# Kernel tuning notes

Hardware: AMD Instinct MI355X
Metric: run time of the kernel (lower is better)

The kernel has to match this reference:

```python
import jax, jax.numpy as jnp
import numpy as np

B, S, HIDDEN = 2, 4096, 4096
NUM_HEADS = 32
QK_NOPE = 128
QK_ROPE = 64
QK_HEAD = QK_NOPE + QK_ROPE
KV_LORA = 512
Q_LORA = 1536


def setup_inputs() -> dict:
    key = jax.random.key(0)
    k1, k2, k3, k4, k5, k6 = jax.random.split(key, 6)
    x = jax.random.normal(k1, (B, S, HIDDEN), dtype=jnp.float32)
    cos = jax.random.uniform(k2, (B, S, QK_ROPE), dtype=jnp.float32)
    sin = jax.random.uniform(k3, (B, S, QK_ROPE), dtype=jnp.float32)
    # Linear weights, torch layout [out, in]
    Wqa = jax.random.normal(k4, (Q_LORA, HIDDEN), dtype=jnp.float32) * 0.02
    Wqb = jax.random.normal(k5, (NUM_HEADS * QK_HEAD, Q_LORA), dtype=jnp.float32) * 0.02
    Wkva = jax.random.normal(k6, (KV_LORA + QK_ROPE, HIDDEN), dtype=jnp.float32) * 0.02
    return {"x": x, "cos": cos, "sin": sin, "Wqa": Wqa, "Wqb": Wqb, "Wkva": Wkva}


def _rotate_half(t):
    d = t.shape[-1] // 2
    return jnp.concatenate([-t[..., d:], t[..., :d]], axis=-1)


def reference(x, cos, sin, Wqa, Wqb, Wkva):
    b, s, _ = x.shape
    # low-rank Q: x -> q_lora -> heads*(nope+rope)
    q = jnp.einsum('bsh,rh->bsr', x, Wqa)
    q = jnp.einsum('bsr,or->bso', q, Wqb).reshape(b, s, NUM_HEADS, QK_HEAD)
    q_nope = q[..., :QK_NOPE]
    q_pe = q[..., QK_NOPE:]
    # KV down-projection with MQA rope part
    kv = jnp.einsum('bsh,oh->bso', x, Wkva)
    compressed_kv = kv[..., :KV_LORA]                         # [b,s,kv_lora]
    k_pe = kv[..., KV_LORA:].reshape(b, s, 1, QK_ROPE)
    # NeoX explicit RoPE, unsqueeze_dim=2
    c = cos[:, :, None, :]
    sn = sin[:, :, None, :]
    q_pe_rot = q_pe * c + _rotate_half(q_pe) * sn
    k_pe_rot = k_pe * c + _rotate_half(k_pe) * sn
    q_out = jnp.concatenate([q_nope, q_pe_rot], axis=-1).reshape(b, s, -1)
    k_out = k_pe_rot.reshape(b, s, QK_ROPE)
    return jnp.concatenate([q_out, k_out, compressed_kv], axis=-1)
```

## Files before the change

kernel.cpp:

```cpp
#include <hip/hip_runtime.h>
#include <hip/hip_bf16.h>
#include <stdint.h>

typedef __bf16 bf16x8 __attribute__((ext_vector_type(8)));
typedef float f32x4 __attribute__((ext_vector_type(4)));
typedef float fvec4 __attribute__((ext_vector_type(4)));
typedef unsigned short usvec4 __attribute__((ext_vector_type(4)));
typedef unsigned int ui32x4 __attribute__((ext_vector_type(4)));

#define AS3 __attribute__((address_space(3)))
#define AS1 __attribute__((address_space(1)))

static __device__ __forceinline__ unsigned short f2bf(float f) {
  unsigned int u = __float_as_uint(f);
  u += 0x7FFF + ((u >> 16) & 1);
  return (unsigned short)(u >> 16);
}


extern "C" __global__ void cvt_bf16_kernel(const float* __restrict__ src,
                                           unsigned short* __restrict__ dst,
                                           long n4) {
  long i = (long)blockIdx.x * blockDim.x + threadIdx.x;
  const long stride = (long)gridDim.x * blockDim.x;
  for (; i < n4; i += stride) {
    const fvec4 v = __builtin_nontemporal_load(&((const fvec4*)src)[i]);
    usvec4 o;
    o.x = f2bf(v.x); o.y = f2bf(v.y); o.z = f2bf(v.z); o.w = f2bf(v.w);
    ((usvec4*)dst)[i] = o;
  }
}

extern "C" __global__ void cvt_pad_kernel(const float* __restrict__ src,
                                          unsigned short* __restrict__ dst,
                                          long nsrc4, long ntot4) {
  long i = (long)blockIdx.x * blockDim.x + threadIdx.x;
  const long stride = (long)gridDim.x * blockDim.x;
  for (; i < ntot4; i += stride) {
    usvec4 o = {0, 0, 0, 0};
    if (i < nsrc4) {
      const fvec4 v = __builtin_nontemporal_load(&((const fvec4*)src)[i]);
      o.x = f2bf(v.x); o.y = f2bf(v.y); o.z = f2bf(v.z); o.w = f2bf(v.w);
    }
    ((usvec4*)dst)[i] = o;
  }
}


#define VMW(N) asm volatile("s_waitcnt vmcnt(" #N ")" ::: "memory")
#define BAR() __builtin_amdgcn_s_barrier()
#define LGKM0() do { asm volatile("s_waitcnt lgkmcnt(0)" ::: "memory"); \
                     __builtin_amdgcn_sched_barrier(0); } while (0)

template <int MODE>
__global__ __launch_bounds__(512, 2)
void mla_gemm(const __hip_bfloat16* __restrict__ A0p,
              const __hip_bfloat16* __restrict__ B0p, int K0,
              const __hip_bfloat16* __restrict__ A1p,
              const __hip_bfloat16* __restrict__ B1p,
              unsigned short* __restrict__ qlora,
              const float* __restrict__ cosp,
              const float* __restrict__ sinp,
              float* __restrict__ out) {
  extern __shared__ __align__(128) char lds[];
  const int tid = threadIdx.x;
  const int lane = tid & 63;
  const int w = tid >> 6;
  const int wm = w >> 2, wn = w & 3;
  const int l15 = lane & 15, lhi = lane >> 4;
  const int srow8 = lane >> 3;
  const int swzc = ((lane & 7) ^ srow8) * 8;

  const __hip_bfloat16* Aptr;
  const __hip_bfloat16* Bptr;
  int K, bm, bn;
  bool isA2 = false;
  if constexpr (MODE == 0) {
    const int swz = ((int)blockIdx.x & 7) * 32 + ((int)blockIdx.x >> 3);
    bm = swz >> 3; bn = swz & 7;
    Aptr = A0p; Bptr = B0p; K = K0;
  } else {
    const int bid = (int)blockIdx.x;
    if (bid < 32) {
      isA2 = true; bm = bid; bn = 8; Aptr = A1p; Bptr = B1p; K = 4096;
    } else {
      const int b2 = bid - 32;
      const int swz = (b2 & 7) * 96 + (b2 >> 3);
      bm = swz / 24; bn = swz - bm * 24;
      Aptr = A0p; Bptr = B0p; K = K0;
    }
  }
  const long brow = (long)bm * 256;
  const int bcol = bn * 256;

  const __hip_bfloat16* aSt = Aptr + (brow + w * 16 + srow8) * (long)K + swzc;
  const __hip_bfloat16* bSt = Bptr + ((long)bcol + srow8) * (long)K + swzc;
  const int wj0 = w * 16, wj1 = w * 16 + 8;
  const int cb_j0 = (2 * (wj0 >> 5)) * 32 + (wj0 & 31);
  const int cb_j1 = (2 * (wj1 >> 5)) * 32 + (wj1 & 31);
  const int ldsWj = w * 2048;

  const int aRdRow = (wm * 64 + l15) * 128;
  const int bRdRow = (wn * 32 + l15) * 128;
  const int ck0 = (lhi ^ (l15 & 7)) * 16;

  f32x4 acc[8][4] = {};
  bf16x8 aF[4][2];
  bf16x8 bF[2][2][2];

  const int T = K >> 6;
  const int I = T >> 1;

  auto stage = [&](int u, int kt) {
    const int b = kt & 1;
    if (u < 2) {
      const int off = b * 32768 + u * 16384 + ldsWj;
      __builtin_amdgcn_global_load_lds((AS1 void*)(aSt + (long)(u * 128) * K + kt * 64),
                                       (AS3 void*)(lds + off), 16, 0, 0);
      __builtin_amdgcn_global_load_lds((AS1 void*)(aSt + (long)(u * 128 + 8) * K + kt * 64),
                                       (AS3 void*)(lds + off + 1024), 16, 0, 0);
    } else {
      const int h = u - 2;
      const int off = 65536 + b * 32768 + h * 16384 + ldsWj;
      __builtin_amdgcn_global_load_lds((AS1 void*)(bSt + (long)(cb_j0 + h * 32) * K + kt * 64),
                                       (AS3 void*)(lds + off), 16, 0, 0);
      __builtin_amdgcn_global_load_lds((AS1 void*)(bSt + (long)(cb_j1 + h * 32) * K + kt * 64),
                                       (AS3 void*)(lds + off + 1024), 16, 0, 0);
    }
  };
  auto readA = [&](int qh, int b) {
    const int base = b * 32768 + qh * 16384 + aRdRow;
    #pragma unroll
    for (int fr = 0; fr < 4; ++fr) {
      aF[fr][0] = *(const bf16x8*)(lds + base + fr * 2048 + ck0);
      aF[fr][1] = *(const bf16x8*)(lds + base + fr * 2048 + (ck0 ^ 64));
    }
  };
  auto readB = [&](int c, int b) {
    const int base = 65536 + b * 32768 + c * 16384 + bRdRow;
    #pragma unroll
    for (int fq = 0; fq < 2; ++fq) {
      bF[c][fq][0] = *(const bf16x8*)(lds + base + fq * 2048 + ck0);
      bF[c][fq][1] = *(const bf16x8*)(lds + base + fq * 2048 + (ck0 ^ 64));
    }
  };
  auto mmac = [&](int qh, int c) {
    __builtin_amdgcn_s_setprio(1);
    #pragma unroll
    for (int fr = 0; fr < 4; ++fr)
      #pragma unroll
      for (int fq = 0; fq < 2; ++fq) {
        acc[qh * 4 + fr][c * 2 + fq] = __builtin_amdgcn_mfma_f32_16x16x32_bf16(
            aF[fr][0], bF[c][fq][0], acc[qh * 4 + fr][c * 2 + fq], 0, 0, 0);
        acc[qh * 4 + fr][c * 2 + fq] = __builtin_amdgcn_mfma_f32_16x16x32_bf16(
            aF[fr][1], bF[c][fq][1], acc[qh * 4 + fr][c * 2 + fq], 0, 0, 0);
      }
    __builtin_amdgcn_s_setprio(0);
  };

  stage(0, 0); stage(2, 0); stage(3, 0); stage(1, 0);
  stage(0, 1); stage(2, 1); stage(3, 1); stage(1, 1);
  VMW(12);
  BAR();

  for (int i = 0; i < I - 1; ++i) {
    const int e2 = 2 * i + 2, o2 = 2 * i + 3;
    readA(0, 0); readB(0, 0);
    BAR(); LGKM0(); mmac(0, 0); VMW(10); BAR();
    readB(1, 0); stage(0, e2); stage(2, e2);
    BAR(); LGKM0(); mmac(0, 1); VMW(12); BAR();
    readA(1, 0); stage(3, e2);
    BAR(); LGKM0(); mmac(1, 1); BAR();
    stage(1, e2);
    BAR(); LGKM0(); mmac(1, 0); VMW(12); BAR();
    readA(0, 1); readB(0, 1);
    BAR(); LGKM0(); mmac(0, 0); VMW(10); BAR();
    readB(1, 1); stage(0, o2); stage(2, o2);
    BAR(); LGKM0(); mmac(0, 1); VMW(12); BAR();
    readA(1, 1); stage(3, o2);
    BAR(); LGKM0(); mmac(1, 1); BAR();
    stage(1, o2);
    BAR(); LGKM0(); mmac(1, 0); VMW(12); BAR();
  }
  readA(0, 0); readB(0, 0);
  BAR(); LGKM0(); mmac(0, 0); VMW(10); BAR();
  readB(1, 0);
  BAR(); LGKM0(); mmac(0, 1); VMW(8); BAR();
  readA(1, 0);
  BAR(); LGKM0(); mmac(1, 1); BAR();
  BAR(); LGKM0(); mmac(1, 0); VMW(4); BAR();
  readA(0, 1); readB(0, 1);
  BAR(); LGKM0(); mmac(0, 0); VMW(2); BAR();
  readB(1, 1);
  BAR(); LGKM0(); mmac(0, 1); VMW(0); BAR();
  readA(1, 1);
  BAR(); LGKM0(); mmac(1, 1); BAR();
  BAR(); LGKM0(); mmac(1, 0); BAR();

  const int wcol = bcol + wn * 64;
  const long rbase = brow + wm * 64;
  char* eplds = lds + w * 4096;

  auto storeTileF32 = [&](int i8, float* dst, bool rope) {
    #pragma unroll
    for (int j = 0; j < 4; ++j)
      #pragma unroll
      for (int r = 0; r < 4; ++r) {
        float v = acc[i8][j][r];
        if (rope) {
          const long row = rbase + (i8 >> 2) * 128 + (i8 & 3) * 16 + lhi * 4 + r;
          const int d = (j >> 1) * 32 + (j & 1) * 16 + l15;
          const float rot = (j < 2) ? -acc[i8][j + 2][r] : acc[i8][j - 2][r];
          v = v * cosp[row * 64 + d] + rot * sinp[row * 64 + d];
        }
        *(float*)(eplds + (lhi * 4 + r) * 256 + ((j >> 1) * 32 + (j & 1) * 16 + l15) * 4) = v;
      }
    asm volatile("s_waitcnt lgkmcnt(0)" ::: "memory");
    #pragma unroll
    for (int t = 0; t < 4; ++t) {
      const int r16 = t * 4 + (lane >> 4);
      const f32x4 v = *(const f32x4*)(eplds + r16 * 256 + (lane & 15) * 16);
      const long row = rbase + (i8 >> 2) * 128 + (i8 & 3) * 16 + r16;
      __builtin_nontemporal_store(v, (f32x4*)(dst + row * 6720 + (lane & 15) * 4));
    }
  };
  auto storeTileBf16 = [&](int i8) {
    #pragma unroll
    for (int j = 0; j < 4; ++j)
      #pragma unroll
      for (int r = 0; r < 4; ++r)
        *(unsigned short*)(eplds + (lhi * 4 + r) * 128 +
                           ((j >> 1) * 32 + (j & 1) * 16 + l15) * 2) = f2bf(acc[i8][j][r]);
    asm volatile("s_waitcnt lgkmcnt(0)" ::: "memory");
    #pragma unroll
    for (int t = 0; t < 2; ++t) {
      const int r16 = t * 8 + (lane >> 3);
      const ui32x4 v = *(const ui32x4*)(eplds + r16 * 128 + (lane & 7) * 16);
      const long row = rbase + (i8 >> 2) * 128 + (i8 & 3) * 16 + r16;
      *(ui32x4*)((char*)qlora + (row * 1536 + wcol) * 2 + (lane & 7) * 16) = v;
    }
  };

  if constexpr (MODE == 0) {
    if (wcol < 1536) {
      #pragma unroll
      for (int i8 = 0; i8 < 8; ++i8) storeTileBf16(i8);
    } else {
      #pragma unroll
      for (int i8 = 0; i8 < 8; ++i8) storeTileF32(i8, out + wcol + 4672, false);
    }
  } else {
    if (isA2) {
      if (wn == 0) {
        #pragma unroll
        for (int i8 = 0; i8 < 8; ++i8) storeTileF32(i8, out + 6144, true);
      }
    } else if ((wcol % 192) != 128) {
      #pragma unroll
      for (int i8 = 0; i8 < 8; ++i8) storeTileF32(i8, out + wcol, false);
    } else {
      #pragma unroll
      for (int i8 = 0; i8 < 8; ++i8) storeTileF32(i8, out + wcol, true);
    }
  }
}


extern "C" void kernel_launch(void* const* d_in, const int* in_sizes, int n_in,
                              void* d_out, int out_size, void* d_ws, size_t ws_size,
                              hipStream_t stream) {
  const float* x    = (const float*)d_in[0];
  const float* cosp = (const float*)d_in[1];
  const float* sinp = (const float*)d_in[2];
  const float* Wqa  = (const float*)d_in[3];
  const float* Wqb  = (const float*)d_in[4];
  const float* Wkva = (const float*)d_in[5];
  float* out = (float*)d_out;

  char* ws = (char*)d_ws;
  __hip_bfloat16* xb  = (__hip_bfloat16*)ws;
  __hip_bfloat16* w1  = (__hip_bfloat16*)(ws + 67108864L);
  __hip_bfloat16* wqb = (__hip_bfloat16*)(ws + 67108864L + 17825792L);
  unsigned short* ql  = (unsigned short*)(ws + 67108864L + 17825792L + 18874368L);

  cvt_bf16_kernel<<<2048, 256, 0, stream>>>(x,   (unsigned short*)xb,  8192L * 4096 / 4);
  cvt_bf16_kernel<<<1024, 256, 0, stream>>>(Wqa, (unsigned short*)w1,  1536L * 4096 / 4);
  cvt_pad_kernel<<<640, 256, 0, stream>>>(Wkva, (unsigned short*)(w1 + 1536L * 4096),
                                          576L * 4096 / 4, 640L * 4096 / 4);
  cvt_bf16_kernel<<<1024, 256, 0, stream>>>(Wqb, (unsigned short*)wqb, 6144L * 1536 / 4);

  (void)hipFuncSetAttribute((const void*)&mla_gemm<0>,
                            hipFuncAttributeMaxDynamicSharedMemorySize, 131072);
  (void)hipFuncSetAttribute((const void*)&mla_gemm<1>,
                            hipFuncAttributeMaxDynamicSharedMemorySize, 131072);

  mla_gemm<0><<<dim3(256), 512, 131072, stream>>>(xb, w1, 4096, nullptr, nullptr,
                                                  ql, cosp, sinp, out);
  mla_gemm<1><<<dim3(800), 512, 131072, stream>>>((const __hip_bfloat16*)ql, wqb, 1536,
                                                  xb, w1, ql, cosp, sinp, out);
}
```

Baseline: 358.4 us.

## Restructure GEMM main loop to one k-tile per iteration with fewer barriers

The unrolled two-k-tile loop body, which had two barriers per MFMA quarter, becomes a per-k-tile loop with roughly one barrier per quarter. LDS reads and global-to-LDS stages are reordered, so the A-half-1 stage for the next tile is issued at the start of the following iteration, with adjusted vmcnt waits. A sched_barrier is added after every s_barrier to keep the compiler from moving instructions across them. This aims to cut synchronization overhead and improve overlap of loads with MFMA, but it risks LDS races if the new wait counts are wrong.

```diff
diff --git a/kernel.cpp b/kernel.cpp
--- a/kernel.cpp
+++ b/kernel.cpp
@@ -48,7 +48,8 @@
 
 
 #define VMW(N) asm volatile("s_waitcnt vmcnt(" #N ")" ::: "memory")
-#define BAR() __builtin_amdgcn_s_barrier()
+#define BAR() do { __builtin_amdgcn_s_barrier(); \
+                   __builtin_amdgcn_sched_barrier(0); } while (0)
 #define LGKM0() do { asm volatile("s_waitcnt lgkmcnt(0)" ::: "memory"); \
                      __builtin_amdgcn_sched_barrier(0); } while (0)
 
@@ -109,7 +110,6 @@
   bf16x8 bF[2][2][2];
 
   const int T = K >> 6;
-  const int I = T >> 1;
 
   auto stage = [&](int u, int kt) {
     const int b = kt & 1;
@@ -163,39 +163,37 @@
   VMW(12);
   BAR();
 
-  for (int i = 0; i < I - 1; ++i) {
-    const int e2 = 2 * i + 2, o2 = 2 * i + 3;
-    readA(0, 0); readB(0, 0);
-    BAR(); LGKM0(); mmac(0, 0); VMW(10); BAR();
-    readB(1, 0); stage(0, e2); stage(2, e2);
-    BAR(); LGKM0(); mmac(0, 1); VMW(12); BAR();
-    readA(1, 0); stage(3, e2);
-    BAR(); LGKM0(); mmac(1, 1); BAR();
-    stage(1, e2);
-    BAR(); LGKM0(); mmac(1, 0); VMW(12); BAR();
-    readA(0, 1); readB(0, 1);
-    BAR(); LGKM0(); mmac(0, 0); VMW(10); BAR();
-    readB(1, 1); stage(0, o2); stage(2, o2);
-    BAR(); LGKM0(); mmac(0, 1); VMW(12); BAR();
-    readA(1, 1); stage(3, o2);
-    BAR(); LGKM0(); mmac(1, 1); BAR();
-    stage(1, o2);
-    BAR(); LGKM0(); mmac(1, 0); VMW(12); BAR();
-  }
-  readA(0, 0); readB(0, 0);
-  BAR(); LGKM0(); mmac(0, 0); VMW(10); BAR();
-  readB(1, 0);
-  BAR(); LGKM0(); mmac(0, 1); VMW(8); BAR();
-  readA(1, 0);
-  BAR(); LGKM0(); mmac(1, 1); BAR();
-  BAR(); LGKM0(); mmac(1, 0); VMW(4); BAR();
-  readA(0, 1); readB(0, 1);
-  BAR(); LGKM0(); mmac(0, 0); VMW(2); BAR();
-  readB(1, 1);
-  BAR(); LGKM0(); mmac(0, 1); VMW(0); BAR();
-  readA(1, 1);
-  BAR(); LGKM0(); mmac(1, 1); BAR();
-  BAR(); LGKM0(); mmac(1, 0); BAR();
+  for (int t = 0; t < T - 2; ++t) {
+    const int b = t & 1;
+    readA(0, b); readB(0, b); if (t) stage(1, t + 1);
+    VMW(10); BAR(); LGKM0(); mmac(0, 0);
+    readB(1, b);
+    VMW(8); BAR(); LGKM0(); mmac(0, 1);
+    readA(1, b); stage(0, t + 2); stage(2, t + 2);
+    BAR(); LGKM0(); mmac(1, 1);
+    stage(3, t + 2);
+    VMW(10); BAR(); mmac(1, 0);
+  }
+  {
+    const int b = (T - 2) & 1;
+    readA(0, b); readB(0, b); stage(1, T - 1);
+    VMW(10); BAR(); LGKM0(); mmac(0, 0);
+    readB(1, b);
+    VMW(8); BAR(); LGKM0(); mmac(0, 1);
+    readA(1, b);
+    BAR(); LGKM0(); mmac(1, 1);
+    VMW(4); BAR(); mmac(1, 0);
+  }
+  {
+    const int b = (T - 1) & 1;
+    readA(0, b); readB(0, b);
+    VMW(2); BAR(); LGKM0(); mmac(0, 0);
+    readB(1, b);
+    VMW(0); BAR(); LGKM0(); mmac(0, 1);
+    readA(1, b);
+    BAR(); LGKM0(); mmac(1, 1);
+    BAR(); mmac(1, 0);
+  }
 
   const int wcol = bcol + wn * 64;
   const long rbase = brow + wm * 64;
```

Result: faster. 341.1 us, median of 2 (-4.8%).
